# Kernel tuning notes

Measured on AMD Instinct MI355X. Metric: run time of the kernel, lower is better.

The kernel has to match this reference:

```python
import jax, jax.numpy as jnp
import numpy as np

EPSILON = 1e-8
TAU = 0.1

def setup_inputs() -> dict:
    key = jax.random.key(0)
    x = jax.random.normal(key, (8192, 256), dtype=jnp.float32)
    return {"x": x}

def reference(x):
    # L2-normalize rows (torch F.normalize: x / max(||x||, 1e-12))
    norm = jnp.maximum(jnp.linalg.norm(x, axis=1, keepdims=True), 1e-12)
    xn = x / norm
    n = xn.shape[0]
    # pairwise cosine similarity via GEMM (equivalent to broadcast sum in source)
    cos = (xn @ xn.T) / TAU                      # [N, N]
    exp_cos = jnp.exp(cos)
    # zero out diagonal (self-similarity)
    exp_cos = exp_cos * (1.0 - jnp.eye(n, dtype=exp_cos.dtype))
    loss = jnp.log(exp_cos.sum(axis=1) / (n - 1) + EPSILON)
    return jnp.mean(loss)
```

## Files before the change

### kernel.cpp

```cpp
#include <hip/hip_runtime.h>
#include <hip/hip_bf16.h>
#include <math.h>

#define TAU_INV_LOG2E 14.4269504088896340736f
#define EPS 1e-8f

typedef __attribute__((ext_vector_type(8))) short bf16x8;
typedef __attribute__((ext_vector_type(4))) float f32x4;

static __device__ __forceinline__ unsigned short f2bf(float f) {
    unsigned int u = __float_as_uint(f);
    unsigned int r = (u + 0x7fffu + ((u >> 16) & 1u)) >> 16;
    return (unsigned short)r;
}

static __device__ __forceinline__ void glds16(const void* g, void* l) {
    __builtin_amdgcn_global_load_lds(
        (const __attribute__((address_space(1))) unsigned int*)g,
        (__attribute__((address_space(3))) unsigned int*)l,
        16, 0, 0);
}

__global__ __launch_bounds__(256) void normalize_kernel(
    const float* __restrict__ x, unsigned short* __restrict__ xn,
    float* __restrict__ rowsum, int N) {
    const int wave = threadIdx.x >> 6;
    const int lane = threadIdx.x & 63;
    const int row  = blockIdx.x * 4 + wave;
    if (row >= N) return;

    if (threadIdx.x < 4) {
        int rr = blockIdx.x * 4 + threadIdx.x;
        if (rr < N) rowsum[rr] = 0.0f;
    }

    const float4 v = ((const float4*)(x + (size_t)row * 256))[lane];
    float s = v.x * v.x + v.y * v.y + v.z * v.z + v.w * v.w;
    s += __shfl_xor(s, 1);
    s += __shfl_xor(s, 2);
    s += __shfl_xor(s, 4);
    s += __shfl_xor(s, 8);
    s += __shfl_xor(s, 16);
    s += __shfl_xor(s, 32);
    const float norm = fmaxf(sqrtf(s), 1e-12f);
    const float rinv = 1.0f / norm;

    ushort4 o;
    o.x = f2bf(v.x * rinv);
    o.y = f2bf(v.y * rinv);
    o.z = f2bf(v.z * rinv);
    o.w = f2bf(v.w * rinv);
    ((ushort4*)(xn + (size_t)row * 256))[lane] = o;
}

__global__ __launch_bounds__(256, 3) void gemm_exp_rowsum_kernel(
    const unsigned short* __restrict__ xn, float* __restrict__ rowsum, int N) {
    const int D = 256;
    __shared__ unsigned short As[2][128 * 32];
    __shared__ unsigned short Bs[2][128 * 32];

    const int tid   = threadIdx.x;
    const int wave  = tid >> 6;
    const int lane  = tid & 63;
    const int waveM = wave >> 1;
    const int waveN = wave & 1;
    const int quad  = lane >> 4;
    const int l16   = lane & 15;

    const int B = N >> 7;
    const int t = blockIdx.x;
    int bi = (int)((2.0 * B + 1.0 -
                    sqrt((2.0 * B + 1.0) * (2.0 * B + 1.0) - 8.0 * (double)t)) * 0.5);
    while (bi > 0 && t < bi * B - (bi * (bi - 1)) / 2) --bi;
    while (t >= (bi + 1) * B - ((bi + 1) * bi) / 2) ++bi;
    const int bj = bi + (t - (bi * B - (bi * (bi - 1)) / 2));
    const bool diag = (bi == bj);

    const int iBase = bi * 128;
    const int jBase = bj * 128;

    f32x4 acc[4][4];
    #pragma unroll
    for (int mt = 0; mt < 4; ++mt)
        #pragma unroll
        for (int nt = 0; nt < 4; ++nt)
            acc[mt][nt] = (f32x4){0.f, 0.f, 0.f, 0.f};

    const int lrow4 = lane >> 2;
    const int csrc  = (lane & 3) ^ ((lane >> 3) & 3);

    auto stage = [&](int buf, int k0) {
        #pragma unroll
        for (int it = 0; it < 2; ++it) {
            const int w = wave * 2 + it;
            const int r = w * 16 + lrow4;
            glds16(xn + (size_t)(iBase + r) * D + k0 + csrc * 8,
                   &As[buf][w * 512]);
            if (!diag)
                glds16(xn + (size_t)(jBase + r) * D + k0 + csrc * 8,
                       &Bs[buf][w * 512]);
        }
    };

    const int swz  = (quad ^ ((l16 >> 1) & 3)) * 8;
    const int offA = (waveM * 64 + l16) * 32 + swz;
    const int offB = (waveN * 64 + l16) * 32 + swz;
    const unsigned short* Bbase = diag ? &As[0][0] : &Bs[0][0];

    stage(0, 0);
    __syncthreads();

    #pragma unroll
    for (int kt = 0; kt < 8; ++kt) {
        const int cb = kt & 1;
        if (kt < 7) stage(cb ^ 1, (kt + 1) * 32);

        const unsigned short* Ap = &As[cb][0];
        const unsigned short* Bp = Bbase + cb * (128 * 32);
        bf16x8 a[4], b[4];
        #pragma unroll
        for (int tt = 0; tt < 4; ++tt) {
            a[tt] = *(const bf16x8*)(Ap + offA + tt * 512);
            b[tt] = *(const bf16x8*)(Bp + offB + tt * 512);
        }
        #pragma unroll
        for (int mt = 0; mt < 4; ++mt)
            #pragma unroll
            for (int nt = 0; nt < 4; ++nt)
                acc[mt][nt] = __builtin_amdgcn_mfma_f32_16x16x32_bf16(
                    a[mt], b[nt], acc[mt][nt], 0, 0, 0);

        if (kt < 7) __syncthreads();
    }

    float rsum[4][4];
    float csum[4] = {0.f, 0.f, 0.f, 0.f};
    #pragma unroll
    for (int mt = 0; mt < 4; ++mt)
        #pragma unroll
        for (int r = 0; r < 4; ++r) rsum[mt][r] = 0.f;

    #pragma unroll
    for (int mt = 0; mt < 4; ++mt) {
        const int gi0 = iBase + waveM * 64 + mt * 16 + quad * 4;
        #pragma unroll
        for (int nt = 0; nt < 4; ++nt) {
            const int gj = jBase + waveN * 64 + nt * 16 + l16;
            #pragma unroll
            for (int r = 0; r < 4; ++r) {
                float e = __builtin_amdgcn_exp2f(acc[mt][nt][r] * TAU_INV_LOG2E);
                if (gi0 + r == gj) e = 0.0f;
                rsum[mt][r] += e;
                csum[nt] += e;
            }
        }
    }
    #pragma unroll
    for (int mt = 0; mt < 4; ++mt) {
        const int gi0 = iBase + waveM * 64 + mt * 16 + quad * 4;
        #pragma unroll
        for (int r = 0; r < 4; ++r) {
            float s = rsum[mt][r];
            s += __shfl_xor(s, 1);
            s += __shfl_xor(s, 2);
            s += __shfl_xor(s, 4);
            s += __shfl_xor(s, 8);
            if (l16 == 0) atomicAdd(&rowsum[gi0 + r], s);
        }
    }
    if (!diag) {
        #pragma unroll
        for (int nt = 0; nt < 4; ++nt) {
            float s = csum[nt];
            s += __shfl_xor(s, 16);
            s += __shfl_xor(s, 32);
            if (quad == 0)
                atomicAdd(&rowsum[jBase + waveN * 64 + nt * 16 + l16], s);
        }
    }
}

__global__ __launch_bounds__(1024) void finalize_kernel(
    const float* __restrict__ rowsum, float* __restrict__ out, int N) {
    __shared__ float red[16];
    const float inv = 1.0f / (float)(N - 1);
    float acc = 0.f;
    const float4* r4 = (const float4*)rowsum;
    for (int i = threadIdx.x; i < (N >> 2); i += 1024) {
        const float4 v = r4[i];
        acc += logf(fmaf(v.x, inv, EPS)) + logf(fmaf(v.y, inv, EPS)) +
               logf(fmaf(v.z, inv, EPS)) + logf(fmaf(v.w, inv, EPS));
    }
    acc += __shfl_xor(acc, 1);
    acc += __shfl_xor(acc, 2);
    acc += __shfl_xor(acc, 4);
    acc += __shfl_xor(acc, 8);
    acc += __shfl_xor(acc, 16);
    acc += __shfl_xor(acc, 32);
    const int wave = threadIdx.x >> 6;
    const int lane = threadIdx.x & 63;
    if (lane == 0) red[wave] = acc;
    __syncthreads();
    if (threadIdx.x == 0) {
        float total = 0.f;
        #pragma unroll
        for (int w = 0; w < 16; ++w) total += red[w];
        out[0] = total / (float)N;
    }
}

extern "C" void kernel_launch(void* const* d_in, const int* in_sizes, int n_in,
                              void* d_out, int out_size, void* d_ws, size_t ws_size,
                              hipStream_t stream) {
    const float* x = (const float*)d_in[0];
    const int D = 256;
    const int N = in_sizes[0] / D;

    unsigned short* xn = (unsigned short*)d_ws;
    float* rowsum = (float*)((char*)d_ws + (size_t)N * D * sizeof(unsigned short));
    float* out = (float*)d_out;

    normalize_kernel<<<(N + 3) / 4, 256, 0, stream>>>(x, xn, rowsum, N);

    const int B = N / 128;
    const int T = B * (B + 1) / 2;
    gemm_exp_rowsum_kernel<<<T, 256, 0, stream>>>(xn, rowsum, N);

    finalize_kernel<<<1, 1024, 0, stream>>>(rowsum, out, N);
}
```

Baseline: 104.1 us.

## Replace rowsum atomics with per-slot partial sums and a parallel finalize

The GEMM epilogue stops issuing float atomicAdds to a shared rowsum array. Each tile instead writes its row and column partial sums into a dedicated slot of a [2B, N] partial buffer indexed by column or row block and wave. The finalize kernel becomes a multi-block reduction: it sums 128 partials per row, takes the log, and atomically adds the block result into the output. This removes atomic contention in the GEMM, at the cost of a larger workspace (128*N floats) and more reads in finalize, and it assumes every slot is written exactly once.

Measured after the change: 95.84 us. 8.0% less time.

```diff
diff --git a/kernel.cpp b/kernel.cpp
--- a/kernel.cpp
+++ b/kernel.cpp
@@ -23,16 +23,13 @@
 
 __global__ __launch_bounds__(256) void normalize_kernel(
     const float* __restrict__ x, unsigned short* __restrict__ xn,
-    float* __restrict__ rowsum, int N) {
+    float* __restrict__ out, int N) {
     const int wave = threadIdx.x >> 6;
     const int lane = threadIdx.x & 63;
     const int row  = blockIdx.x * 4 + wave;
     if (row >= N) return;
 
-    if (threadIdx.x < 4) {
-        int rr = blockIdx.x * 4 + threadIdx.x;
-        if (rr < N) rowsum[rr] = 0.0f;
-    }
+    if (blockIdx.x == 0 && threadIdx.x == 0) out[0] = 0.0f;
 
     const float4 v = ((const float4*)(x + (size_t)row * 256))[lane];
     float s = v.x * v.x + v.y * v.y + v.z * v.z + v.w * v.w;
@@ -54,7 +51,7 @@
 }
 
 __global__ __launch_bounds__(256, 3) void gemm_exp_rowsum_kernel(
-    const unsigned short* __restrict__ xn, float* __restrict__ rowsum, int N) {
+    const unsigned short* __restrict__ xn, float* __restrict__ prow, int N) {
     const int D = 256;
     __shared__ unsigned short As[2][128 * 32];
     __shared__ unsigned short Bs[2][128 * 32];
@@ -155,42 +152,44 @@
             }
         }
     }
-    #pragma unroll
-    for (int mt = 0; mt < 4; ++mt) {
-        const int gi0 = iBase + waveM * 64 + mt * 16 + quad * 4;
-        #pragma unroll
-        for (int r = 0; r < 4; ++r) {
-            float s = rsum[mt][r];
-            s += __shfl_xor(s, 1);
-            s += __shfl_xor(s, 2);
-            s += __shfl_xor(s, 4);
-            s += __shfl_xor(s, 8);
-            if (l16 == 0) atomicAdd(&rowsum[gi0 + r], s);
+    {
+        float* slot = prow + (size_t)(2 * bj + waveN) * N;
+        #pragma unroll
+        for (int mt = 0; mt < 4; ++mt) {
+            const int gi0 = iBase + waveM * 64 + mt * 16 + quad * 4;
+            #pragma unroll
+            for (int r = 0; r < 4; ++r) {
+                float s = rsum[mt][r];
+                s += __shfl_xor(s, 1);
+                s += __shfl_xor(s, 2);
+                s += __shfl_xor(s, 4);
+                s += __shfl_xor(s, 8);
+                if (l16 == 0) slot[gi0 + r] = s;
+            }
         }
     }
     if (!diag) {
+        float* slot = prow + (size_t)(2 * bi + waveM) * N;
         #pragma unroll
         for (int nt = 0; nt < 4; ++nt) {
             float s = csum[nt];
             s += __shfl_xor(s, 16);
             s += __shfl_xor(s, 32);
             if (quad == 0)
-                atomicAdd(&rowsum[jBase + waveN * 64 + nt * 16 + l16], s);
-        }
-    }
-}
-
-__global__ __launch_bounds__(1024) void finalize_kernel(
-    const float* __restrict__ rowsum, float* __restrict__ out, int N) {
-    __shared__ float red[16];
+                slot[jBase + waveN * 64 + nt * 16 + l16] = s;
+        }
+    }
+}
+
+__global__ __launch_bounds__(256) void finalize_kernel(
+    const float* __restrict__ prow, float* __restrict__ out, int N) {
+    __shared__ float red[4];
+    const int i = blockIdx.x * 256 + threadIdx.x;
     const float inv = 1.0f / (float)(N - 1);
-    float acc = 0.f;
-    const float4* r4 = (const float4*)rowsum;
-    for (int i = threadIdx.x; i < (N >> 2); i += 1024) {
-        const float4 v = r4[i];
-        acc += logf(fmaf(v.x, inv, EPS)) + logf(fmaf(v.y, inv, EPS)) +
-               logf(fmaf(v.z, inv, EPS)) + logf(fmaf(v.w, inv, EPS));
-    }
+    float s = 0.f;
+    #pragma unroll 16
+    for (int p = 0; p < 128; ++p) s += prow[(size_t)p * N + i];
+    float acc = logf(fmaf(s, inv, EPS));
     acc += __shfl_xor(acc, 1);
     acc += __shfl_xor(acc, 2);
     acc += __shfl_xor(acc, 4);
@@ -202,10 +201,8 @@
     if (lane == 0) red[wave] = acc;
     __syncthreads();
     if (threadIdx.x == 0) {
-        float total = 0.f;
-        #pragma unroll
-        for (int w = 0; w < 16; ++w) total += red[w];
-        out[0] = total / (float)N;
+        float total = red[0] + red[1] + red[2] + red[3];
+        atomicAdd(out, total / (float)N);
     }
 }
 
@@ -217,14 +214,14 @@
     const int N = in_sizes[0] / D;
 
     unsigned short* xn = (unsigned short*)d_ws;
-    float* rowsum = (float*)((char*)d_ws + (size_t)N * D * sizeof(unsigned short));
+    float* prow = (float*)((char*)d_ws + (size_t)N * D * sizeof(unsigned short));
     float* out = (float*)d_out;
 
-    normalize_kernel<<<(N + 3) / 4, 256, 0, stream>>>(x, xn, rowsum, N);
+    normalize_kernel<<<(N + 3) / 4, 256, 0, stream>>>(x, xn, out, N);
 
     const int B = N / 128;
     const int T = B * (B + 1) / 2;
-    gemm_exp_rowsum_kernel<<<T, 256, 0, stream>>>(xn, rowsum, N);
-
-    finalize_kernel<<<1, 1024, 0, stream>>>(rowsum, out, N);
-}
+    gemm_exp_rowsum_kernel<<<T, 256, 0, stream>>>(xn, prow, N);
+
+    finalize_kernel<<<N / 256, 256, 0, stream>>>(prow, out, N);
+}
```
